# Performance work log

Hardware: AMD Instinct MI355X
Metric: run time of the kernel (lower is better)

## Reference

```python
import jax, jax.numpy as jnp
import numpy as np

N_NODES = 50000
N_EDGES = 800000
IN_DIM = 128
NUM_GRAPHS = 64
NEG_SLOPE = 0.2  # PyG GATConv default


def _gat_layer(x, src, dst, W, a_s, a_d, b):
    """PyG GATConv (concat=True), eval mode (no dropout).
    x: [N, Fin]; W: [H*C, Fin]; a_s, a_d: [H, C]; b: [H*C]."""
    N = x.shape[0]
    H, C = a_s.shape
    h = (x @ W.T).reshape(N, H, C)                      # [N,H,C]
    es = jnp.einsum('nhc,hc->nh', h, a_s)               # [N,H]
    ed = jnp.einsum('nhc,hc->nh', h, a_d)               # [N,H]
    e = jax.nn.leaky_relu(es[src] + ed[dst], NEG_SLOPE)  # [E,H]
    # segment softmax over incoming edges of each destination node
    m = jax.ops.segment_max(e, dst, num_segments=N)     # [N,H]
    ex = jnp.exp(e - m[dst])
    denom = jax.ops.segment_sum(ex, dst, num_segments=N)
    alpha = ex / denom[dst]                             # [E,H]
    out = jax.ops.segment_sum(h[src] * alpha[:, :, None], dst, num_segments=N)
    return out.reshape(N, H * C) + b


def _make_params(key):
    dims = [(512, IN_DIM, 8, 64), (256, 512, 8, 32), (128, 256, 8, 16), (512, 128, 8, 64)]
    ps = {}
    k = key
    for i, (out_f, in_f, H, C) in enumerate(dims, 1):
        k, k1, k2, k3 = jax.random.split(k, 4)
        s = 1.0 / np.sqrt(in_f)
        ps[f'W{i}'] = jax.random.normal(k1, (out_f, in_f), jnp.float32) * s
        ps[f'a{i}s'] = jax.random.normal(k2, (H, C), jnp.float32) * 0.1
        ps[f'a{i}d'] = jax.random.normal(k3, (H, C), jnp.float32) * 0.1
        ps[f'b{i}'] = jnp.zeros((out_f,), jnp.float32)
    k, k1, k2 = jax.random.split(k, 3)
    ps['lw1'] = jax.random.normal(k1, (32, 512), jnp.float32) * (1.0 / np.sqrt(512))
    ps['lb1'] = jnp.zeros((32,), jnp.float32)
    ps['lw2'] = jax.random.normal(k2, (2, 32), jnp.float32) * (1.0 / np.sqrt(32))
    ps['lb2'] = jnp.zeros((2,), jnp.float32)
    return ps


def setup_inputs() -> dict:
    key = jax.random.key(0)
    kx, ke, kb, kp = jax.random.split(key, 4)
    x = jax.random.normal(kx, (N_NODES, IN_DIM), jnp.float32)
    edge_index = jax.random.randint(ke, (2, N_EDGES), 0, N_NODES, jnp.int64 if jax.config.jax_enable_x64 else jnp.int32)
    batch = jnp.sort(jax.random.randint(kb, (N_NODES,), 0, NUM_GRAPHS, edge_index.dtype))
    inp = {'x': x, 'edge_index': edge_index, 'batch': batch}
    inp.update(_make_params(kp))
    return inp


def reference(x, edge_index, batch,
              W1, a1s, a1d, b1, W2, a2s, a2d, b2,
              W3, a3s, a3d, b3, W4, a4s, a4d, b4,
              lw1, lb1, lw2, lb2):
    N = x.shape[0]
    # PyG GATConv add_self_loops=True
    loop = jnp.arange(N, dtype=edge_index.dtype)
    src = jnp.concatenate([edge_index[0], loop])
    dst = jnp.concatenate([edge_index[1], loop])

    h = jax.nn.elu(_gat_layer(x, src, dst, W1, a1s, a1d, b1))
    h = jax.nn.elu(_gat_layer(h, src, dst, W2, a2s, a2d, b2))
    h = jax.nn.elu(_gat_layer(h, src, dst, W3, a3s, a3d, b3))
    h = _gat_layer(h, src, dst, W4, a4s, a4d, b4)

    # global mean pool over graphs
    sums = jax.ops.segment_sum(h, batch, num_segments=NUM_GRAPHS)
    cnts = jax.ops.segment_sum(jnp.ones((N, 1), h.dtype), batch, num_segments=NUM_GRAPHS)
    g = sums / jnp.maximum(cnts, 1.0)                   # [G, 512]

    g = jax.nn.elu(g @ lw1.T + lb1)                     # dropout skipped (eval)
    return g @ lw2.T + lb2                              # [G, 2]
```

## Files before the change

kernel.cpp:

```cpp
#include <hip/hip_runtime.h>
#include <math.h>

#define NN 50000
#define NE 800000
#define NEP (NE + NN)
#define NGR 64
#define NHEAD 8
#define MPAD 50048
#define KSTASH 6

typedef short short8 __attribute__((ext_vector_type(8)));
typedef float floatx4 __attribute__((ext_vector_type(4)));
typedef unsigned uintx4 __attribute__((ext_vector_type(4)));

__device__ inline float bf2f(short s) {
    union { unsigned u; float f; } v;
    v.u = ((unsigned)(unsigned short)s) << 16;
    return v.f;
}
__device__ inline float bf2f_lo(unsigned p) {
    union { unsigned u; float f; } v; v.u = p << 16; return v.f;
}
__device__ inline float bf2f_hi(unsigned p) {
    union { unsigned u; float f; } v; v.u = p & 0xffff0000u; return v.f;
}
__device__ inline short f2bf(float f) {
    union { float f; unsigned u; } v; v.f = f;
    unsigned r = v.u + 0x7fffu + ((v.u >> 16) & 1u);
    return (short)(r >> 16);
}

__device__ inline void gl_lds16(const short* g, short* l) {
    __builtin_amdgcn_global_load_lds(
        (const __attribute__((address_space(1))) unsigned int*)g,
        (__attribute__((address_space(3))) unsigned int*)l, 16, 0, 0);
}

__global__ void count_deg(const int* __restrict__ ei, int* __restrict__ deg) {
    int e = blockIdx.x * 256 + threadIdx.x;
    if (e >= NEP) return;
    int d = (e < NE) ? ei[NE + e] : (e - NE);
    atomicAdd(&deg[d], 1);
}

__global__ __launch_bounds__(1024) void scan_local(const int* __restrict__ deg,
                                                   int* __restrict__ out,
                                                   int* __restrict__ bsum, int n) {
    __shared__ int sd[1024];
    int b = blockIdx.x, t = threadIdx.x;
    int i = b * 1024 + t;
    int v = (i < n) ? deg[i] : 0;
    sd[t] = v;
    __syncthreads();
    for (int off = 1; off < 1024; off <<= 1) {
        int tmp = (t >= off) ? sd[t - off] : 0;
        __syncthreads();
        sd[t] += tmp;
        __syncthreads();
    }
    if (i < n) out[i] = sd[t] - v;
    if (t == 1023) bsum[b] = sd[1023];
}

__global__ void scan_bsum(int* __restrict__ bsum, int nb) {
    if (threadIdx.x == 0) {
        int s = 0;
        for (int i = 0; i < nb; i++) { int v = bsum[i]; bsum[i] = s; s += v; }
        bsum[nb] = s;
    }
}

__global__ void scan_add(int* __restrict__ row_ptr, int* __restrict__ cursor,
                         const int* __restrict__ bsum, int n, int nb) {
    int i = blockIdx.x * 256 + threadIdx.x;
    if (i < n) {
        int v = row_ptr[i] + bsum[i >> 10];
        row_ptr[i] = v;
        cursor[i] = v;
    } else if (i == n) {
        row_ptr[n] = bsum[nb];
    }
}

__global__ void scatter_edges(const int* __restrict__ ei, int* __restrict__ cursor,
                              int* __restrict__ srcs) {
    int e = blockIdx.x * 256 + threadIdx.x;
    if (e >= NEP) return;
    int s, d;
    if (e < NE) { s = ei[e]; d = ei[NE + e]; }
    else        { s = e - NE; d = e - NE; }
    int pos = atomicAdd(&cursor[d], 1);
    srcs[pos] = s;
}

__global__ void conv_w_all(const float* __restrict__ w0, const float* __restrict__ w1,
                           const float* __restrict__ w2, const float* __restrict__ w3,
                           short* __restrict__ out) {
    int i = blockIdx.x * 256 + threadIdx.x;
    if (i >= 294912) return;
    const float* src; int off;
    if (i < 65536)       { src = w0; off = i; }
    else if (i < 196608) { src = w1; off = i - 65536; }
    else if (i < 229376) { src = w2; off = i - 196608; }
    else                 { src = w3; off = i - 229376; }
    out[i] = f2bf(src[off]);
}

__global__ void conv_x_pad4(const float* __restrict__ x, short* __restrict__ xb) {
    int i = blockIdx.x * 256 + threadIdx.x;
    if (i >= MPAD * 32) return;
    int r = i >> 5;
    short4 o;
    if (r < NN) {
        float4 v = *(const float4*)&x[(size_t)i * 4];
        o.x = f2bf(v.x); o.y = f2bf(v.y); o.z = f2bf(v.z); o.w = f2bf(v.w);
    } else {
        o.x = o.y = o.z = o.w = 0;
    }
    *(short4*)&xb[(size_t)i * 4] = o;
}

template <int C>
__global__ __launch_bounds__(256) void gemm_bf(const short* __restrict__ A,
                                               const short* __restrict__ B,
                                               short* __restrict__ Cout,
                                               const float* __restrict__ a_s,
                                               const float* __restrict__ a_d,
                                               float* __restrict__ es,
                                               float* __restrict__ ed,
                                               int K) {
    constexpr int Nc = 8 * C;
    constexpr int colTiles = Nc / 128;
    constexpr int JPH = C / 16;
    constexpr int HPW = 64 / C;
    __shared__ __align__(16) short As[128 * 64];
    __shared__ __align__(16) short Bs[128 * 64];
    int bx = blockIdx.x % colTiles;
    int by = blockIdx.x / colTiles;
    int row0 = by * 128, col0 = bx * 128;
    int t = threadIdx.x;
    int lane = t & 63, w = t >> 6;
    int wr = (w >> 1) * 64, wc = (w & 1) * 64;
    int lrow = lane & 15, lq = lane >> 4;

    int srow = lane >> 3;
    int kcsrc = (lane & 7) ^ srow;

    floatx4 acc[4][4];
#pragma unroll
    for (int i = 0; i < 4; i++)
#pragma unroll
        for (int j = 0; j < 4; j++) acc[i][j] = (floatx4)0.0f;

    for (int k0 = 0; k0 < K; k0 += 64) {
#pragma unroll
        for (int it = 0; it < 4; it++) {
            int r0 = w * 32 + it * 8;
            int r = r0 + srow;
            gl_lds16(&A[(size_t)(row0 + r) * K + k0 + kcsrc * 8], &As[r0 * 64]);
            gl_lds16(&B[(size_t)(col0 + r) * K + k0 + kcsrc * 8], &Bs[r0 * 64]);
        }
        __syncthreads();
#pragma unroll
        for (int kk = 0; kk < 2; kk++) {
            int slot = (kk * 4 + lq) ^ (lrow & 7);
            short8 af[4], bfr[4];
#pragma unroll
            for (int i = 0; i < 4; i++)
                af[i] = *(const short8*)&As[(wr + i * 16 + lrow) * 64 + slot * 8];
#pragma unroll
            for (int j = 0; j < 4; j++)
                bfr[j] = *(const short8*)&Bs[(wc + j * 16 + lrow) * 64 + slot * 8];
#pragma unroll
            for (int i = 0; i < 4; i++)
#pragma unroll
                for (int j = 0; j < 4; j++)
                    acc[i][j] = __builtin_amdgcn_mfma_f32_16x16x32_bf16(af[i], bfr[j], acc[i][j], 0, 0, 0);
        }
        __syncthreads();
    }

#pragma unroll
    for (int i = 0; i < 4; i++)
#pragma unroll
        for (int j = 0; j < 4; j++)
#pragma unroll
            for (int r = 0; r < 4; r++) {
                int row = row0 + wr + i * 16 + lq * 4 + r;
                int col = col0 + wc + j * 16 + lrow;
                Cout[(size_t)row * Nc + col] = f2bf(acc[i][j][r]);
            }

    float asv[4], adv[4];
#pragma unroll
    for (int j = 0; j < 4; j++) {
        int colA = col0 + wc + j * 16 + lrow;
        asv[j] = a_s[colA];
        adv[j] = a_d[colA];
    }
    int hb = (col0 + wc) / C;
#pragma unroll
    for (int i = 0; i < 4; i++)
#pragma unroll
        for (int r = 0; r < 4; r++) {
            float s_h[HPW], d_h[HPW];
#pragma unroll
            for (int hh = 0; hh < HPW; hh++) { s_h[hh] = 0.f; d_h[hh] = 0.f; }
#pragma unroll
            for (int j = 0; j < 4; j++) {
                s_h[j / JPH] = fmaf(acc[i][j][r], asv[j], s_h[j / JPH]);
                d_h[j / JPH] = fmaf(acc[i][j][r], adv[j], d_h[j / JPH]);
            }
#pragma unroll
            for (int hh = 0; hh < HPW; hh++) {
#pragma unroll
                for (int off = 1; off <= 8; off <<= 1) {
                    s_h[hh] += __shfl_xor(s_h[hh], off);
                    d_h[hh] += __shfl_xor(d_h[hh], off);
                }
            }
            if (lrow == 0) {
                int row = row0 + wr + i * 16 + lq * 4 + r;
                if (row < NN) {
#pragma unroll
                    for (int hh = 0; hh < HPW; hh++) {
                        es[row * 8 + hb + hh] = s_h[hh];
                        ed[row * 8 + hb + hh] = d_h[hh];
                    }
                }
            }
        }
}

__global__ __launch_bounds__(256) void alpha_kernel(const float* __restrict__ es,
                                                    const float* __restrict__ ed,
                                                    const int* __restrict__ row_ptr,
                                                    const int* __restrict__ srcs,
                                                    float* __restrict__ alpha) {
    int wave = threadIdx.x >> 6, lane = threadIdx.x & 63;
    int n = __builtin_amdgcn_readfirstlane(blockIdx.x * 4 + wave);
    int start = row_ptr[n];
    int deg = row_ptr[n + 1] - start;
    int m8 = deg * 8;
    const int* sp = srcs + start;
    float* ap = alpha + start;
    int hh = lane & 7;
    int hoff = hh * NEP;
    float edv = ed[n * 8 + hh];
    float st[KSTASH];
    float pm = -1e30f, ps = 0.f;
#pragma unroll
    for (int i = 0; i < KSTASH; i++) {
        int idx = lane + i * 64;
        if (idx < m8) {
            int s = sp[idx >> 3];
            float e = es[s * 8 + hh] + edv;
            e = e > 0.f ? e : 0.2f * e;
            st[i] = e;
            float mn = fmaxf(pm, e);
            ps = ps * __expf(pm - mn) + __expf(e - mn);
            pm = mn;
        }
    }
    for (int idx = lane + KSTASH * 64; idx < m8; idx += 64) {
        int s = sp[idx >> 3];
        float e = es[s * 8 + hh] + edv;
        e = e > 0.f ? e : 0.2f * e;
        float mn = fmaxf(pm, e);
        ps = ps * __expf(pm - mn) + __expf(e - mn);
        pm = mn;
    }
#pragma unroll
    for (int off = 8; off <= 32; off <<= 1) {
        float mo = __shfl_xor(pm, off);
        float so = __shfl_xor(ps, off);
        float mn = fmaxf(pm, mo);
        ps = ps * __expf(pm - mn) + so * __expf(mo - mn);
        pm = mn;
    }
    float invd = 1.0f / ps;
#pragma unroll
    for (int i = 0; i < KSTASH; i++) {
        int idx = lane + i * 64;
        if (idx < m8) ap[hoff + (idx >> 3)] = __expf(st[i] - pm) * invd;
    }
    for (int idx = lane + KSTASH * 64; idx < m8; idx += 64) {
        int s = sp[idx >> 3];
        float e = es[s * 8 + hh] + edv;
        e = e > 0.f ? e : 0.2f * e;
        ap[hoff + (idx >> 3)] = __expf(e - pm) * invd;
    }
}

template <int C, bool ELU>
__global__ __launch_bounds__(256) void aggr_chunk(const short* __restrict__ h,
                                                  const float* __restrict__ alpha,
                                                  const int* __restrict__ row_ptr,
                                                  const int* __restrict__ srcs,
                                                  const float* __restrict__ bias,
                                                  short* __restrict__ out) {
    constexpr int HC = NHEAD * C;
    constexpr int NCH = HC / 64;
    constexpr int NPW = 4;
    constexpr int RSH = (C == 64) ? 10 : (C == 32) ? 9 : 8;
    int chunk = blockIdx.x % NCH;
    int grp   = blockIdx.x / NCH;
    int wave = threadIdx.x >> 6, lane = threadIdx.x & 63;
    int sub = lane & 7;
    int g   = lane >> 3;
    int c0 = chunk * 64 + sub * 8;
    unsigned c02 = (unsigned)(c0 * 2);
    int head = c0 / C;
    int hoff = head * NEP;
    int nbase = (grp * 4 + wave) * NPW;
    for (int ni = 0; ni < NPW; ni++) {
        int n = __builtin_amdgcn_readfirstlane(nbase + ni);
        int start = row_ptr[n];
        int deg = row_ptr[n + 1] - start;
        const int* sp = srcs + start;
        const float* ap = alpha + start;
        int nit = deg >> 4;
        float acc[8];
#pragma unroll
        for (int j = 0; j < 8; j++) acc[j] = 0.f;
        int kb = g;
        for (int it = 0; it < nit; ++it, kb += 16) {
            int s0 = sp[kb];
            int s1 = sp[kb + 8];
            float w0 = ap[hoff + kb];
            float w1 = ap[hoff + kb + 8];
            uintx4 h0 = *(const uintx4*)((const char*)h + (((unsigned)s0 << RSH) + c02));
            uintx4 h1 = *(const uintx4*)((const char*)h + (((unsigned)s1 << RSH) + c02));
#pragma unroll
            for (int j = 0; j < 4; j++) {
                acc[2 * j]     = fmaf(w0, bf2f_lo(h0[j]), acc[2 * j]);
                acc[2 * j + 1] = fmaf(w0, bf2f_hi(h0[j]), acc[2 * j + 1]);
            }
#pragma unroll
            for (int j = 0; j < 4; j++) {
                acc[2 * j]     = fmaf(w1, bf2f_lo(h1[j]), acc[2 * j]);
                acc[2 * j + 1] = fmaf(w1, bf2f_hi(h1[j]), acc[2 * j + 1]);
            }
        }
        for (int k = kb; k < deg; k += 8) {
            int s0 = sp[k];
            float w0 = ap[hoff + k];
            uintx4 h0 = *(const uintx4*)((const char*)h + (((unsigned)s0 << RSH) + c02));
#pragma unroll
            for (int j = 0; j < 4; j++) {
                acc[2 * j]     = fmaf(w0, bf2f_lo(h0[j]), acc[2 * j]);
                acc[2 * j + 1] = fmaf(w0, bf2f_hi(h0[j]), acc[2 * j + 1]);
            }
        }
#pragma unroll
        for (int j = 0; j < 8; j++) {
            acc[j] += __shfl_xor(acc[j], 8);
            acc[j] += __shfl_xor(acc[j], 16);
            acc[j] += __shfl_xor(acc[j], 32);
        }
        if (lane < 8) {
            int cc = chunk * 64 + lane * 8;
            floatx4 b0 = *(const floatx4*)&bias[cc];
            floatx4 b1 = *(const floatx4*)&bias[cc + 4];
            float bb[8] = {b0[0], b0[1], b0[2], b0[3], b1[0], b1[1], b1[2], b1[3]};
            unsigned pk[4];
#pragma unroll
            for (int j = 0; j < 4; j++) {
                float o0 = acc[2 * j] + bb[2 * j];
                float o1 = acc[2 * j + 1] + bb[2 * j + 1];
                if (ELU) {
                    o0 = o0 > 0.f ? o0 : (__expf(o0) - 1.0f);
                    o1 = o1 > 0.f ? o1 : (__expf(o1) - 1.0f);
                }
                pk[j] = ((unsigned)(unsigned short)f2bf(o0)) |
                        (((unsigned)(unsigned short)f2bf(o1)) << 16);
            }
            *(uintx4*)&out[(size_t)n * HC + cc] = *(uintx4*)pk;
        }
    }
}

__global__ __launch_bounds__(256) void pool_kernel(const short* __restrict__ h,
                                                   const int* __restrict__ batch,
                                                   float* __restrict__ gout) {
    __shared__ float red[4 * 64];
    int g = blockIdx.x >> 3;
    int fc = (blockIdx.x & 7) * 64;
    int lo = 0, hi = NN;
    while (lo < hi) { int mid = (lo + hi) >> 1; if (batch[mid] < g) lo = mid + 1; else hi = mid; }
    int s = lo;
    lo = 0; hi = NN;
    while (lo < hi) { int mid = (lo + hi) >> 1; if (batch[mid] < g + 1) lo = mid + 1; else hi = mid; }
    int e = lo;
    int t = threadIdx.x;
    int wave = t >> 6, lane = t & 63;
    int f8 = (lane & 7) * 8;
    int stripe = wave * 8 + (lane >> 3);
    float acc[8];
#pragma unroll
    for (int j = 0; j < 8; j++) acc[j] = 0.f;
    for (int r = s + stripe; r < e; r += 32) {
        short8 v = *(const short8*)&h[(size_t)r * 512 + fc + f8];
#pragma unroll
        for (int j = 0; j < 8; j++) acc[j] += bf2f(v[j]);
    }
#pragma unroll
    for (int j = 0; j < 8; j++) {
        acc[j] += __shfl_xor(acc[j], 8);
        acc[j] += __shfl_xor(acc[j], 16);
        acc[j] += __shfl_xor(acc[j], 32);
    }
    if (lane < 8) {
#pragma unroll
        for (int j = 0; j < 8; j++) red[wave * 64 + lane * 8 + j] = acc[j];
    }
    __syncthreads();
    if (t < 64) {
        float v = red[t] + red[64 + t] + red[128 + t] + red[192 + t];
        float inv = 1.0f / fmaxf((float)(e - s), 1.0f);
        gout[g * 512 + fc + t] = v * inv;
    }
}

__global__ __launch_bounds__(64) void mlp_kernel(const float* __restrict__ g,
                                                 const float* __restrict__ lw1,
                                                 const float* __restrict__ lb1,
                                                 const float* __restrict__ lw2,
                                                 const float* __restrict__ lb2,
                                                 float* __restrict__ outp) {
    __shared__ float gv[512];
    __shared__ float y1[32];
    int b = blockIdx.x, t = threadIdx.x;
    for (int i = t; i < 512; i += 64) gv[i] = g[b * 512 + i];
    __syncthreads();
    if (t < 32) {
        float a = lb1[t];
        for (int k = 0; k < 512; k++) a = fmaf(gv[k], lw1[t * 512 + k], a);
        y1[t] = a > 0.f ? a : (__expf(a) - 1.0f);
    }
    __syncthreads();
    if (t < 2) {
        float a = lb2[t];
        for (int k = 0; k < 32; k++) a = fmaf(y1[k], lw2[t * 32 + k], a);
        outp[b * 2 + t] = a;
    }
}

extern "C" void kernel_launch(void* const* d_in, const int* in_sizes, int n_in,
                              void* d_out, int out_size, void* d_ws, size_t ws_size,
                              hipStream_t stream) {
    (void)in_sizes; (void)n_in; (void)out_size; (void)ws_size;
    const float* x     = (const float*)d_in[0];
    const int*   ei    = (const int*)d_in[1];
    const int*   batch = (const int*)d_in[2];
    const float* W[4]  = {(const float*)d_in[3], (const float*)d_in[7],
                          (const float*)d_in[11], (const float*)d_in[15]};
    const float* As_[4] = {(const float*)d_in[4], (const float*)d_in[8],
                           (const float*)d_in[12], (const float*)d_in[16]};
    const float* Ad_[4] = {(const float*)d_in[5], (const float*)d_in[9],
                           (const float*)d_in[13], (const float*)d_in[17]};
    const float* Bi[4]  = {(const float*)d_in[6], (const float*)d_in[10],
                           (const float*)d_in[14], (const float*)d_in[18]};
    const float* lw1 = (const float*)d_in[19];
    const float* lb1 = (const float*)d_in[20];
    const float* lw2 = (const float*)d_in[21];
    const float* lb2 = (const float*)d_in[22];
    float* out = (float*)d_out;

    short* Ab = (short*)d_ws;
    short* Hb = Ab + (size_t)MPAD * 512;
    short* Wb = Hb + (size_t)MPAD * 512;
    short* Wb_[4] = {Wb, Wb + 65536, Wb + 196608, Wb + 229376};
    float* esb  = (float*)(Wb + 294912);
    float* edb  = esb + NN * NHEAD;
    float* gbuf = edb + NN * NHEAD;
    int* row_ptr = (int*)(gbuf + NGR * 512);
    int* cursor  = row_ptr + (NN + 1);
    int* srcs    = cursor + (NN + 1);
    int* bsum    = srcs + NEP;
    float* alphab = (float*)(bsum + 64);

    const int nblk = (NN + 1023) / 1024;

    hipMemsetAsync(cursor, 0, NN * sizeof(int), stream);
    count_deg<<<(NEP + 255) / 256, 256, 0, stream>>>(ei, cursor);
    scan_local<<<nblk, 1024, 0, stream>>>(cursor, row_ptr, bsum, NN);
    scan_bsum<<<1, 64, 0, stream>>>(bsum, nblk);
    scan_add<<<(NN + 256) / 256, 256, 0, stream>>>(row_ptr, cursor, bsum, NN, nblk);
    scatter_edges<<<(NEP + 255) / 256, 256, 0, stream>>>(ei, cursor, srcs);

    conv_x_pad4<<<(MPAD * 32 + 255) / 256, 256, 0, stream>>>(x, Ab);
    conv_w_all<<<(294912 + 255) / 256, 256, 0, stream>>>(W[0], W[1], W[2], W[3], Wb);

    const int rowTiles = MPAD / 128;
    const int ag  = NN / 4;
    const int ngp = NN / 16;

    gemm_bf<64><<<rowTiles * 4, 256, 0, stream>>>(Ab, Wb_[0], Hb, As_[0], Ad_[0], esb, edb, 128);
    alpha_kernel<<<ag, 256, 0, stream>>>(esb, edb, row_ptr, srcs, alphab);
    aggr_chunk<64, true><<<ngp * 8, 256, 0, stream>>>(Hb, alphab, row_ptr, srcs, Bi[0], Ab);

    gemm_bf<32><<<rowTiles * 2, 256, 0, stream>>>(Ab, Wb_[1], Hb, As_[1], Ad_[1], esb, edb, 512);
    alpha_kernel<<<ag, 256, 0, stream>>>(esb, edb, row_ptr, srcs, alphab);
    aggr_chunk<32, true><<<ngp * 4, 256, 0, stream>>>(Hb, alphab, row_ptr, srcs, Bi[1], Ab);

    gemm_bf<16><<<rowTiles * 1, 256, 0, stream>>>(Ab, Wb_[2], Hb, As_[2], Ad_[2], esb, edb, 256);
    alpha_kernel<<<ag, 256, 0, stream>>>(esb, edb, row_ptr, srcs, alphab);
    aggr_chunk<16, true><<<ngp * 2, 256, 0, stream>>>(Hb, alphab, row_ptr, srcs, Bi[2], Ab);

    gemm_bf<64><<<rowTiles * 4, 256, 0, stream>>>(Ab, Wb_[3], Hb, As_[3], Ad_[3], esb, edb, 128);
    alpha_kernel<<<ag, 256, 0, stream>>>(esb, edb, row_ptr, srcs, alphab);
    aggr_chunk<64, false><<<ngp * 8, 256, 0, stream>>>(Hb, alphab, row_ptr, srcs, Bi[3], Ab);

    pool_kernel<<<NGR * 8, 256, 0, stream>>>(Ab, batch, gbuf);
    mlp_kernel<<<NGR, 64, 0, stream>>>(gbuf, lw1, lb1, lw2, lb2, out);
}
```

Baseline: 844.6 us.

## Map one node per 8-lane group in aggregation instead of splitting edges across lanes

The aggregation kernel used to give each wave 4 nodes processed one after another, with the 8 lane-groups splitting each node's edge list and then combining through cross-lane shuffles. Now each 8-lane group owns its own destination node and walks that node's full edge list, so a wave handles 8 nodes at once and no shuffle reduction is needed. This removes the shuffle and serial per-node overhead, but lanes in a wave now diverge on differing node degrees (about 17 on average). Loads of srcs and alpha are no longer coalesced across the groups within a node.

```diff
diff --git a/kernel.cpp b/kernel.cpp
--- a/kernel.cpp
+++ b/kernel.cpp
@@ -293,90 +293,82 @@
 }
 
 template <int C, bool ELU>
-__global__ __launch_bounds__(256) void aggr_chunk(const short* __restrict__ h,
-                                                  const float* __restrict__ alpha,
-                                                  const int* __restrict__ row_ptr,
-                                                  const int* __restrict__ srcs,
-                                                  const float* __restrict__ bias,
-                                                  short* __restrict__ out) {
+__global__ __launch_bounds__(256) void aggr_npg(const short* __restrict__ h,
+                                                const float* __restrict__ alpha,
+                                                const int* __restrict__ row_ptr,
+                                                const int* __restrict__ srcs,
+                                                const float* __restrict__ bias,
+                                                short* __restrict__ out) {
     constexpr int HC = NHEAD * C;
     constexpr int NCH = HC / 64;
-    constexpr int NPW = 4;
     constexpr int RSH = (C == 64) ? 10 : (C == 32) ? 9 : 8;
     int chunk = blockIdx.x % NCH;
     int grp   = blockIdx.x / NCH;
-    int wave = threadIdx.x >> 6, lane = threadIdx.x & 63;
+    int lane = threadIdx.x & 63;
+    int wave = threadIdx.x >> 6;
     int sub = lane & 7;
     int g   = lane >> 3;
+    int n = grp * 32 + wave * 8 + g;
     int c0 = chunk * 64 + sub * 8;
     unsigned c02 = (unsigned)(c0 * 2);
     int head = c0 / C;
-    int hoff = head * NEP;
-    int nbase = (grp * 4 + wave) * NPW;
-    for (int ni = 0; ni < NPW; ni++) {
-        int n = __builtin_amdgcn_readfirstlane(nbase + ni);
-        int start = row_ptr[n];
-        int deg = row_ptr[n + 1] - start;
-        const int* sp = srcs + start;
-        const float* ap = alpha + start;
-        int nit = deg >> 4;
-        float acc[8];
-#pragma unroll
-        for (int j = 0; j < 8; j++) acc[j] = 0.f;
-        int kb = g;
-        for (int it = 0; it < nit; ++it, kb += 16) {
-            int s0 = sp[kb];
-            int s1 = sp[kb + 8];
-            float w0 = ap[hoff + kb];
-            float w1 = ap[hoff + kb + 8];
-            uintx4 h0 = *(const uintx4*)((const char*)h + (((unsigned)s0 << RSH) + c02));
-            uintx4 h1 = *(const uintx4*)((const char*)h + (((unsigned)s1 << RSH) + c02));
-#pragma unroll
-            for (int j = 0; j < 4; j++) {
-                acc[2 * j]     = fmaf(w0, bf2f_lo(h0[j]), acc[2 * j]);
-                acc[2 * j + 1] = fmaf(w0, bf2f_hi(h0[j]), acc[2 * j + 1]);
+    bool valid = n < NN;
+    int start = 0, deg = 0;
+    if (valid) {
+        start = row_ptr[n];
+        deg = row_ptr[n + 1] - start;
+    }
+    unsigned soff = (unsigned)start;
+    unsigned aoff = (unsigned)(head * NEP + start);
+    float acc[8];
+#pragma unroll
+    for (int j = 0; j < 8; j++) acc[j] = 0.f;
+    int k = 0;
+    for (; k + 1 < deg; k += 2) {
+        int s0 = srcs[soff + k];
+        int s1 = srcs[soff + k + 1];
+        float w0 = alpha[aoff + k];
+        float w1 = alpha[aoff + k + 1];
+        uintx4 h0 = *(const uintx4*)((const char*)h + (((unsigned)s0 << RSH) + c02));
+        uintx4 h1 = *(const uintx4*)((const char*)h + (((unsigned)s1 << RSH) + c02));
+#pragma unroll
+        for (int j = 0; j < 4; j++) {
+            acc[2 * j]     = fmaf(w0, bf2f_lo(h0[j]), acc[2 * j]);
+            acc[2 * j + 1] = fmaf(w0, bf2f_hi(h0[j]), acc[2 * j + 1]);
+        }
+#pragma unroll
+        for (int j = 0; j < 4; j++) {
+            acc[2 * j]     = fmaf(w1, bf2f_lo(h1[j]), acc[2 * j]);
+            acc[2 * j + 1] = fmaf(w1, bf2f_hi(h1[j]), acc[2 * j + 1]);
+        }
+    }
+    if (k < deg) {
+        int s0 = srcs[soff + k];
+        float w0 = alpha[aoff + k];
+        uintx4 h0 = *(const uintx4*)((const char*)h + (((unsigned)s0 << RSH) + c02));
+#pragma unroll
+        for (int j = 0; j < 4; j++) {
+            acc[2 * j]     = fmaf(w0, bf2f_lo(h0[j]), acc[2 * j]);
+            acc[2 * j + 1] = fmaf(w0, bf2f_hi(h0[j]), acc[2 * j + 1]);
+        }
+    }
+    if (valid) {
+        floatx4 b0 = *(const floatx4*)&bias[c0];
+        floatx4 b1 = *(const floatx4*)&bias[c0 + 4];
+        float bb[8] = {b0[0], b0[1], b0[2], b0[3], b1[0], b1[1], b1[2], b1[3]};
+        unsigned pk[4];
+#pragma unroll
+        for (int j = 0; j < 4; j++) {
+            float o0 = acc[2 * j] + bb[2 * j];
+            float o1 = acc[2 * j + 1] + bb[2 * j + 1];
+            if (ELU) {
+                o0 = o0 > 0.f ? o0 : (__expf(o0) - 1.0f);
+                o1 = o1 > 0.f ? o1 : (__expf(o1) - 1.0f);
             }
-#pragma unroll
-            for (int j = 0; j < 4; j++) {
-                acc[2 * j]     = fmaf(w1, bf2f_lo(h1[j]), acc[2 * j]);
-                acc[2 * j + 1] = fmaf(w1, bf2f_hi(h1[j]), acc[2 * j + 1]);
-            }
-        }
-        for (int k = kb; k < deg; k += 8) {
-            int s0 = sp[k];
-            float w0 = ap[hoff + k];
-            uintx4 h0 = *(const uintx4*)((const char*)h + (((unsigned)s0 << RSH) + c02));
-#pragma unroll
-            for (int j = 0; j < 4; j++) {
-                acc[2 * j]     = fmaf(w0, bf2f_lo(h0[j]), acc[2 * j]);
-                acc[2 * j + 1] = fmaf(w0, bf2f_hi(h0[j]), acc[2 * j + 1]);
-            }
-        }
-#pragma unroll
-        for (int j = 0; j < 8; j++) {
-            acc[j] += __shfl_xor(acc[j], 8);
-            acc[j] += __shfl_xor(acc[j], 16);
-            acc[j] += __shfl_xor(acc[j], 32);
-        }
-        if (lane < 8) {
-            int cc = chunk * 64 + lane * 8;
-            floatx4 b0 = *(const floatx4*)&bias[cc];
-            floatx4 b1 = *(const floatx4*)&bias[cc + 4];
-            float bb[8] = {b0[0], b0[1], b0[2], b0[3], b1[0], b1[1], b1[2], b1[3]};
-            unsigned pk[4];
-#pragma unroll
-            for (int j = 0; j < 4; j++) {
-                float o0 = acc[2 * j] + bb[2 * j];
-                float o1 = acc[2 * j + 1] + bb[2 * j + 1];
-                if (ELU) {
-                    o0 = o0 > 0.f ? o0 : (__expf(o0) - 1.0f);
-                    o1 = o1 > 0.f ? o1 : (__expf(o1) - 1.0f);
-                }
-                pk[j] = ((unsigned)(unsigned short)f2bf(o0)) |
-                        (((unsigned)(unsigned short)f2bf(o1)) << 16);
-            }
-            *(uintx4*)&out[(size_t)n * HC + cc] = *(uintx4*)pk;
-        }
+            pk[j] = ((unsigned)(unsigned short)f2bf(o0)) |
+                    (((unsigned)(unsigned short)f2bf(o1)) << 16);
+        }
+        *(uintx4*)&out[(size_t)n * HC + c0] = *(uintx4*)pk;
     }
 }
 
@@ -494,23 +486,23 @@
 
     const int rowTiles = MPAD / 128;
     const int ag  = NN / 4;
-    const int ngp = NN / 16;
+    const int ngb = (NN + 31) / 32;
 
     gemm_bf<64><<<rowTiles * 4, 256, 0, stream>>>(Ab, Wb_[0], Hb, As_[0], Ad_[0], esb, edb, 128);
     alpha_kernel<<<ag, 256, 0, stream>>>(esb, edb, row_ptr, srcs, alphab);
-    aggr_chunk<64, true><<<ngp * 8, 256, 0, stream>>>(Hb, alphab, row_ptr, srcs, Bi[0], Ab);
+    aggr_npg<64, true><<<ngb * 8, 256, 0, stream>>>(Hb, alphab, row_ptr, srcs, Bi[0], Ab);
 
     gemm_bf<32><<<rowTiles * 2, 256, 0, stream>>>(Ab, Wb_[1], Hb, As_[1], Ad_[1], esb, edb, 512);
     alpha_kernel<<<ag, 256, 0, stream>>>(esb, edb, row_ptr, srcs, alphab);
-    aggr_chunk<32, true><<<ngp * 4, 256, 0, stream>>>(Hb, alphab, row_ptr, srcs, Bi[1], Ab);
+    aggr_npg<32, true><<<ngb * 4, 256, 0, stream>>>(Hb, alphab, row_ptr, srcs, Bi[1], Ab);
 
     gemm_bf<16><<<rowTiles * 1, 256, 0, stream>>>(Ab, Wb_[2], Hb, As_[2], Ad_[2], esb, edb, 256);
     alpha_kernel<<<ag, 256, 0, stream>>>(esb, edb, row_ptr, srcs, alphab);
-    aggr_chunk<16, true><<<ngp * 2, 256, 0, stream>>>(Hb, alphab, row_ptr, srcs, Bi[2], Ab);
+    aggr_npg<16, true><<<ngb * 2, 256, 0, stream>>>(Hb, alphab, row_ptr, srcs, Bi[2], Ab);
 
     gemm_bf<64><<<rowTiles * 4, 256, 0, stream>>>(Ab, Wb_[3], Hb, As_[3], Ad_[3], esb, edb, 128);
     alpha_kernel<<<ag, 256, 0, stream>>>(esb, edb, row_ptr, srcs, alphab);
-    aggr_chunk<64, false><<<ngp * 8, 256, 0, stream>>>(Hb, alphab, row_ptr, srcs, Bi[3], Ab);
+    aggr_npg<64, false><<<ngb * 8, 256, 0, stream>>>(Hb, alphab, row_ptr, srcs, Bi[3], Ab);
 
     pool_kernel<<<NGR * 8, 256, 0, stream>>>(Ab, batch, gbuf);
     mlp_kernel<<<NGR, 64, 0, stream>>>(gbuf, lw1, lb1, lw2, lb2, out);
```

Result: faster. 776.2 us (-8.1%).
